# Optimization experiments

Hardware: AMD Instinct MI355X
Metric: run time of the kernel (lower is better)

## Reference

```python
import jax, jax.numpy as jnp
import numpy as np

B = 16384
D_IN = 4096        # must equal N_FEATURES for the original code to be shape-consistent
N_FEATURES = 4096
K = 128


def setup_inputs() -> dict:
    key = jax.random.key(0)
    kx, kw = jax.random.split(key)
    x = jax.random.normal(kx, (B, D_IN), dtype=jnp.float32)
    preencoder_bias = jnp.zeros((D_IN,), dtype=jnp.float32)
    # kaiming_uniform-like init: bound = sqrt(6 / fan_in)
    bound = float(np.sqrt(6.0 / D_IN))
    W_enc = jax.random.uniform(kw, (N_FEATURES, D_IN), dtype=jnp.float32,
                               minval=-bound, maxval=bound)
    b_enc = jnp.zeros((N_FEATURES,), dtype=jnp.float32)
    return {"x": x, "preencoder_bias": preencoder_bias, "W_enc": W_enc, "b_enc": b_enc}


def reference(x, preencoder_bias, W_enc, b_enc):
    # y = (x - preencoder_bias) @ W_enc + b_enc   (W_enc is square: d_in == n_features)
    xc = x - preencoder_bias                      # [B, d_in]
    y = xc @ W_enc + b_enc                        # [B, n_features]
    acts = jax.nn.relu(y)
    # top-k threshold masking: keep entries >= k-th largest per row (ties included)
    topk_vals = jax.lax.top_k(acts, K)[0]         # [B, K], sorted descending
    threshold = topk_vals[..., -1:]               # [B, 1]
    return acts * (acts >= threshold)
```

## Files before the change

### kernel.cpp

```cpp
#include <hip/hip_runtime.h>
#include <hip/hip_bf16.h>


typedef __bf16  bf16x8 __attribute__((ext_vector_type(8)));
typedef float   f32x4  __attribute__((ext_vector_type(4)));

__device__ __forceinline__ unsigned short f2bf(float f) {
    __hip_bfloat16 h = __float2bfloat16(f);
    return __builtin_bit_cast(unsigned short, h);
}
__device__ __forceinline__ float bf2f(unsigned short u) {
    __hip_bfloat16 h = __builtin_bit_cast(__hip_bfloat16, u);
    return __bfloat162float(h);
}

#define GLL16(g, l)                                                          \
    __builtin_amdgcn_global_load_lds(                                        \
        (const __attribute__((address_space(1))) unsigned int*)(g),          \
        (__attribute__((address_space(3))) unsigned int*)(l), 16, 0, 0)

__global__ __launch_bounds__(256)
void presplit_x(const float* __restrict__ x, const float* __restrict__ pb,
                unsigned short* __restrict__ Xhi, unsigned short* __restrict__ Xlo,
                int Kdim, size_t total) {
    size_t base = ((size_t)blockIdx.x * 256 + threadIdx.x) * 8;
    if (base >= total) return;
    int kcol = (int)(base % Kdim);
    __align__(16) unsigned short hi[8], lo[8];
    #pragma unroll
    for (int q = 0; q < 2; ++q) {
        float4 xv = *(const float4*)&x[base + q * 4];
        float4 pv = *(const float4*)&pb[kcol + q * 4];
        float v[4] = {xv.x - pv.x, xv.y - pv.y, xv.z - pv.z, xv.w - pv.w};
        #pragma unroll
        for (int r = 0; r < 4; ++r) {
            hi[q*4+r] = f2bf(v[r]);
            lo[q*4+r] = f2bf(v[r] - bf2f(hi[q*4+r]));
        }
    }
    *(uint4*)&Xhi[base] = *(uint4*)&hi[0];
    *(uint4*)&Xlo[base] = *(uint4*)&lo[0];
}

__global__ __launch_bounds__(256)
void split_transpose_W(const float* __restrict__ W,
                       unsigned short* __restrict__ Wt_hi,
                       unsigned short* __restrict__ Wt_lo,
                       int N, int Kdim) {
    __shared__ float tile[64][65];
    const int tx = threadIdx.x;
    const int nB = blockIdx.x * 64;
    const int kB = blockIdx.y * 64;

    #pragma unroll
    for (int p = 0; p < 4; ++p) {
        int e  = tx + 256 * p;
        int kl = e >> 4;
        int n4 = (e & 15) << 2;
        float4 v = *(const float4*)&W[(size_t)(kB + kl) * N + nB + n4];
        tile[kl][n4 + 0] = v.x; tile[kl][n4 + 1] = v.y;
        tile[kl][n4 + 2] = v.z; tile[kl][n4 + 3] = v.w;
    }
    __syncthreads();

    #pragma unroll
    for (int p = 0; p < 4; ++p) {
        int e  = tx + 256 * p;
        int nl = e >> 4;
        int k4 = (e & 15) << 2;
        unsigned short hi[4], lo[4];
        #pragma unroll
        for (int r = 0; r < 4; ++r) {
            float f = tile[k4 + r][nl];
            hi[r] = f2bf(f);
            lo[r] = f2bf(f - bf2f(hi[r]));
        }
        size_t off = (size_t)(nB + nl) * Kdim + kB + k4;
        *(ushort4*)&Wt_hi[off] = *(ushort4*)&hi[0];
        *(ushort4*)&Wt_lo[off] = *(ushort4*)&lo[0];
    }
}

__global__ __launch_bounds__(512, 2)
void gemm_presplit_i(const unsigned short* __restrict__ Xhi,
                     const unsigned short* __restrict__ Xlo,
                     const unsigned short* __restrict__ Wt_hi,
                     const unsigned short* __restrict__ Wt_lo,
                     const float* __restrict__ be,
                     float* __restrict__ out, int M, int N, int Kdim) {
    __shared__ unsigned short sA[2][256 * 64];
    __shared__ unsigned short sB[2][256 * 64];

    const int tx   = threadIdx.x;
    const int lane = tx & 63;
    const int wv   = tx >> 6;
    const int ln   = lane & 15;
    const int quad = lane >> 4;
    const int wm   = wv >> 2;
    const int wn   = wv & 3;

    const int mT = M >> 8, nT = N >> 8, total = mT * nT;
    int wgid = blockIdx.y * gridDim.x + blockIdx.x;
    int xcd = wgid & 7, idx = wgid >> 3;
    int qq = total >> 3, rr_ = total & 7;
    int swz = (xcd < rr_ ? xcd * (qq + 1) : rr_ * (qq + 1) + (xcd - rr_) * qq) + idx;
    const int mBase = (swz / nT) << 8;
    const int nBase = (swz % nT) << 8;

    const int rr  = tx >> 3;
    const int lc8 = tx & 7;
    const int lgc = lc8 ^ (rr & 7);
    const unsigned short* aSrc = (lgc & 4) ? Xlo : Xhi;
    const unsigned short* bSrc = (lgc & 4) ? Wt_lo : Wt_hi;
    const int srcoff = (lgc & 3) << 3;
    const int arow_b = (rr & 31) + ((rr & 32) << 2);

    const int pA = (quad ^ (ln & 7)) << 3;

#define STAGE_B(bufp, r, k0_) do {                                            \
        int row_ = ((r) << 6) + rr;                                           \
        GLL16(bSrc + (size_t)(nBase + row_) * Kdim + (k0_) + srcoff,          \
              &sB[bufp][(row_ << 6) + (lc8 << 3)]);                           \
    } while (0)
#define STAGE_A(bufp, r, k0_) do {                                            \
        int row_ = ((r) << 5) + arow_b;                                       \
        GLL16(aSrc + (size_t)(mBase + row_) * Kdim + (k0_) + srcoff,          \
              &sA[bufp][(row_ << 6) + (lc8 << 3)]);                           \
    } while (0)

    f32x4 acc[8][4] = {};

    const int NT = Kdim >> 5;

    STAGE_B(0, 0, 0); STAGE_B(0, 1, 0); STAGE_B(0, 2, 0); STAGE_B(0, 3, 0);
    STAGE_A(0, 0, 0); STAGE_A(0, 1, 0); STAGE_A(0, 2, 0); STAGE_A(0, 3, 0);
    asm volatile("s_waitcnt vmcnt(0)" ::: "memory");
    __builtin_amdgcn_s_barrier();
    __builtin_amdgcn_sched_barrier(0);

    for (int t = 0; t < NT; ++t) {
        const int cur = t & 1, nxt = cur ^ 1;
        const bool more = (t + 1 < NT);
        const int k1 = (t + 1) << 5;

        bf16x8 bhi[4], blo[4];
        #pragma unroll
        for (int q = 0; q < 4; ++q) {
            if (q == 0) {
                #pragma unroll
                for (int j = 0; j < 4; ++j) {
                    int rb = wn * 64 + j * 16 + ln;
                    bhi[j] = *(const bf16x8*)&sB[cur][(rb << 6) + pA];
                    blo[j] = *(const bf16x8*)&sB[cur][(rb << 6) + (pA ^ 32)];
                }
            }
            bf16x8 ahi[2], alo[2];
            #pragma unroll
            for (int ii = 0; ii < 2; ++ii) {
                int ra = wm * 128 + (2 * q + ii) * 16 + ln;
                ahi[ii] = *(const bf16x8*)&sA[cur][(ra << 6) + pA];
                alo[ii] = *(const bf16x8*)&sA[cur][(ra << 6) + (pA ^ 32)];
            }

            if (more) {
                if (q == 0)      { STAGE_B(nxt, 0, k1); STAGE_B(nxt, 1, k1); }
                else if (q == 1) { STAGE_B(nxt, 2, k1); STAGE_B(nxt, 3, k1); }
                else if (q == 2) { STAGE_A(nxt, 0, k1); STAGE_A(nxt, 1, k1); }
                else             { STAGE_A(nxt, 2, k1); STAGE_A(nxt, 3, k1); }
            }

            __builtin_amdgcn_s_barrier();
            __builtin_amdgcn_s_setprio(1);
            #pragma unroll
            for (int ii = 0; ii < 2; ++ii)
                #pragma unroll
                for (int j = 0; j < 4; ++j)
                    acc[2 * q + ii][j] = __builtin_amdgcn_mfma_f32_16x16x32_bf16(
                        ahi[ii], bhi[j], acc[2 * q + ii][j], 0, 0, 0);
            #pragma unroll
            for (int ii = 0; ii < 2; ++ii)
                #pragma unroll
                for (int j = 0; j < 4; ++j)
                    acc[2 * q + ii][j] = __builtin_amdgcn_mfma_f32_16x16x32_bf16(
                        ahi[ii], blo[j], acc[2 * q + ii][j], 0, 0, 0);
            #pragma unroll
            for (int ii = 0; ii < 2; ++ii)
                #pragma unroll
                for (int j = 0; j < 4; ++j)
                    acc[2 * q + ii][j] = __builtin_amdgcn_mfma_f32_16x16x32_bf16(
                        alo[ii], bhi[j], acc[2 * q + ii][j], 0, 0, 0);
            __builtin_amdgcn_s_setprio(0);

            if (more) {
                if (q == 0)      asm volatile("s_waitcnt vmcnt(4)" ::: "memory");
                else if (q == 1) asm volatile("s_waitcnt vmcnt(5)" ::: "memory");
                else if (q == 2) asm volatile("s_waitcnt vmcnt(6)" ::: "memory");
                else             asm volatile("s_waitcnt vmcnt(3)" ::: "memory");
            } else {
                if (q == 0)      asm volatile("s_waitcnt vmcnt(2)" ::: "memory");
                else if (q == 1) asm volatile("s_waitcnt vmcnt(1)" ::: "memory");
                else if (q == 2) asm volatile("s_waitcnt vmcnt(0)" ::: "memory");
            }
            __builtin_amdgcn_s_barrier();
            __builtin_amdgcn_sched_barrier(0);
        }
    }

    #pragma unroll
    for (int j = 0; j < 4; ++j) {
        int n = nBase + wn * 64 + j * 16 + ln;
        float bev = be[n];
        #pragma unroll
        for (int i = 0; i < 8; ++i) {
            #pragma unroll
            for (int r = 0; r < 4; ++r) {
                int m = mBase + wm * 128 + i * 16 + quad * 4 + r;
                out[(size_t)m * N + n] = fmaxf(acc[i][j][r] + bev, 0.f);
            }
        }
    }
#undef STAGE_B
#undef STAGE_A
}

__global__ __launch_bounds__(256)
void gemm_split_bf16(const float* __restrict__ x, const float* __restrict__ pb,
                     const unsigned short* __restrict__ Wt_hi,
                     const unsigned short* __restrict__ Wt_lo,
                     const float* __restrict__ be,
                     float* __restrict__ out, int M, int N, int Kdim) {
    __shared__ unsigned short sAhi[128][32];
    __shared__ unsigned short sAlo[128][32];
    __shared__ unsigned short sBhi[128][32];
    __shared__ unsigned short sBlo[128][32];

    const int tx    = threadIdx.x;
    const int nBase = blockIdx.x * 128;
    const int mBase = blockIdx.y * 128;
    const int wv    = tx >> 6;
    const int lane  = tx & 63;
    const int ln    = lane & 15;
    const int quad  = lane >> 4;
    const int wm    = wv >> 1;
    const int wn    = wv & 1;
    const int am = tx >> 1;
    const int ak = (tx & 1) * 16;
    const int bn  = wv * 16 + (lane >> 2);
    const int bk8 = (lane & 3) * 8;

    f32x4 acc[4][4] = {};

    for (int k0 = 0; k0 < Kdim; k0 += 32) {
        __syncthreads();
        #pragma unroll
        for (int r = 0; r < 2; ++r) {
            int nrow = r * 64 + bn;
            size_t goff = (size_t)(nBase + nrow) * Kdim + k0 + bk8;
            GLL16(&Wt_hi[goff], &sBhi[nrow][bk8]);
            GLL16(&Wt_lo[goff], &sBlo[nrow][bk8]);
        }
        {
            const float* xrow = x  + (size_t)(mBase + am) * Kdim + k0 + ak;
            const float* pbp  = pb + k0 + ak;
            float v[16];
            #pragma unroll
            for (int q = 0; q < 4; ++q) {
                float4 xv = *(const float4*)(xrow + q * 4);
                float4 pv = *(const float4*)(pbp + q * 4);
                v[q*4+0] = xv.x - pv.x; v[q*4+1] = xv.y - pv.y;
                v[q*4+2] = xv.z - pv.z; v[q*4+3] = xv.w - pv.w;
            }
            __align__(16) unsigned short hi[16], lo[16];
            #pragma unroll
            for (int q = 0; q < 16; ++q) {
                hi[q] = f2bf(v[q]);
                lo[q] = f2bf(v[q] - bf2f(hi[q]));
            }
            *(uint4*)&sAhi[am][ak]     = *(uint4*)&hi[0];
            *(uint4*)&sAhi[am][ak + 8] = *(uint4*)&hi[8];
            *(uint4*)&sAlo[am][ak]     = *(uint4*)&lo[0];
            *(uint4*)&sAlo[am][ak + 8] = *(uint4*)&lo[8];
        }
        __syncthreads();

        bf16x8 ahi[4], alo[4], bhi[4], blo[4];
        #pragma unroll
        for (int i = 0; i < 4; ++i) {
            int m = wm * 64 + i * 16 + ln;
            ahi[i] = *(const bf16x8*)&sAhi[m][quad * 8];
            alo[i] = *(const bf16x8*)&sAlo[m][quad * 8];
        }
        #pragma unroll
        for (int j = 0; j < 4; ++j) {
            int n = wn * 64 + j * 16 + ln;
            bhi[j] = *(const bf16x8*)&sBhi[n][quad * 8];
            blo[j] = *(const bf16x8*)&sBlo[n][quad * 8];
        }
        #pragma unroll
        for (int i = 0; i < 4; ++i)
            #pragma unroll
            for (int j = 0; j < 4; ++j) {
                acc[i][j] = __builtin_amdgcn_mfma_f32_16x16x32_bf16(ahi[i], bhi[j], acc[i][j], 0, 0, 0);
                acc[i][j] = __builtin_amdgcn_mfma_f32_16x16x32_bf16(ahi[i], blo[j], acc[i][j], 0, 0, 0);
                acc[i][j] = __builtin_amdgcn_mfma_f32_16x16x32_bf16(alo[i], bhi[j], acc[i][j], 0, 0, 0);
            }
    }

    #pragma unroll
    for (int j = 0; j < 4; ++j) {
        int n = nBase + wn * 64 + j * 16 + ln;
        float bev = be[n];
        #pragma unroll
        for (int i = 0; i < 4; ++i)
            #pragma unroll
            for (int r = 0; r < 4; ++r) {
                int m = mBase + wm * 64 + i * 16 + quad * 4 + r;
                out[(size_t)m * N + n] = fmaxf(acc[i][j][r] + bev, 0.f);
            }
    }
}

#define BAND    2e-4f
#define AMB_CAP 64

__global__ __launch_bounds__(256)
void topk_mask_exact(const float* __restrict__ x, const float* __restrict__ pb,
                     const float* __restrict__ W, const float* __restrict__ be,
                     float* __restrict__ out, int N, int Kdim, int Ksel) {
    __shared__ int    s_red[4];
    __shared__ int    s_nhi, s_namb;
    __shared__ int    amb_idx[AMB_CAP];
    __shared__ double amb_d[AMB_CAP];
    __shared__ int    amb_keep[AMB_CAP];
    __shared__ double dred[4];

    const int tx  = threadIdx.x;
    const int row = blockIdx.x;
    float* rowp = out + (size_t)row * N;

    float v[16];
    #pragma unroll
    for (int p = 0; p < 4; ++p) {
        float4 f = *(const float4*)&rowp[(tx + 256 * p) << 2];
        v[p*4+0] = f.x; v[p*4+1] = f.y; v[p*4+2] = f.z; v[p*4+3] = f.w;
    }
    unsigned uv[16];
    #pragma unroll
    for (int i = 0; i < 16; ++i) uv[i] = __float_as_uint(v[i]);

    int c0 = 0;
    #pragma unroll
    for (int i = 0; i < 16; ++i) c0 += (uv[i] != 0u) ? 1 : 0;
    #pragma unroll
    for (int off = 32; off > 0; off >>= 1) c0 += __shfl_down(c0, off);
    if ((tx & 63) == 0) s_red[tx >> 6] = c0;
    __syncthreads();
    const int total_nz = s_red[0] + s_red[1] + s_red[2] + s_red[3];

    unsigned thr_u = 0;
    if (total_nz >= Ksel) {
        unsigned blo_ = 1u, bhi_ = 0x7f7fffffu;
        while (blo_ < bhi_) {
            unsigned mid = blo_ + ((bhi_ - blo_ + 1) >> 1);
            int cc = 0;
            #pragma unroll
            for (int i = 0; i < 16; ++i) cc += (uv[i] >= mid) ? 1 : 0;
            #pragma unroll
            for (int off = 32; off > 0; off >>= 1) cc += __shfl_down(cc, off);
            __syncthreads();
            if ((tx & 63) == 0) s_red[tx >> 6] = cc;
            __syncthreads();
            int cnt = s_red[0] + s_red[1] + s_red[2] + s_red[3];
            if (cnt >= Ksel) blo_ = mid; else bhi_ = mid - 1;
        }
        thr_u = blo_;
    }
    const float thr = __uint_as_float(thr_u);

    if (thr < 0.01f) {
        #pragma unroll
        for (int p = 0; p < 4; ++p) {
            float4 o;
            o.x = (v[p*4+0] >= thr) ? v[p*4+0] : 0.f;
            o.y = (v[p*4+1] >= thr) ? v[p*4+1] : 0.f;
            o.z = (v[p*4+2] >= thr) ? v[p*4+2] : 0.f;
            o.w = (v[p*4+3] >= thr) ? v[p*4+3] : 0.f;
            *(float4*)&rowp[(tx + 256 * p) << 2] = o;
        }
        return;
    }

    if (tx == 0) { s_nhi = 0; s_namb = 0; }
    __syncthreads();

    int my_hi = 0;
    #pragma unroll
    for (int i = 0; i < 16; ++i) {
        float val = v[i];
        if (val > thr + BAND) my_hi++;
        else if (val >= thr - BAND) {
            int slot = atomicAdd(&s_namb, 1);
            if (slot < AMB_CAP) amb_idx[slot] = ((tx + 256 * (i >> 2)) << 2) + (i & 3);
        }
    }
    atomicAdd(&s_nhi, my_hi);
    __syncthreads();

    const int nhi   = s_nhi;
    const int namb  = (s_namb < AMB_CAP) ? s_namb : AMB_CAP;
    const int kneed = Ksel - nhi;
    const bool fallback = (s_namb > AMB_CAP) || (kneed < 0) || (kneed > s_namb);

    if (fallback) {
        #pragma unroll
        for (int p = 0; p < 4; ++p) {
            float4 o;
            o.x = (v[p*4+0] >= thr) ? v[p*4+0] : 0.f;
            o.y = (v[p*4+1] >= thr) ? v[p*4+1] : 0.f;
            o.z = (v[p*4+2] >= thr) ? v[p*4+2] : 0.f;
            o.w = (v[p*4+3] >= thr) ? v[p*4+3] : 0.f;
            *(float4*)&rowp[(tx + 256 * p) << 2] = o;
        }
        return;
    }

    if (namb > kneed) {
        for (int j = 0; j < namb; ++j) {
            const int n = amb_idx[j];
            double partial = 0.0;
            for (int p = 0; p < Kdim / 256; ++p) {
                int k = tx + 256 * p;
                partial += ((double)x[(size_t)row * Kdim + k] - (double)pb[k]) *
                           (double)W[(size_t)k * N + n];
            }
            #pragma unroll
            for (int off = 32; off > 0; off >>= 1) partial += __shfl_down(partial, off);
            if ((tx & 63) == 0) dred[tx >> 6] = partial;
            __syncthreads();
            if (tx == 0) amb_d[j] = dred[0] + dred[1] + dred[2] + dred[3] + (double)be[n];
            __syncthreads();
        }
        if (tx == 0) {
            for (int j = 0; j < namb; ++j) {
                int greater = 0;
                for (int l = 0; l < namb; ++l)
                    if (amb_d[l] > amb_d[j]) greater++;
                amb_keep[j] = (greater < kneed) ? 1 : 0;
            }
        }
        __syncthreads();
    } else {
        for (int j = tx; j < namb; j += 256) amb_keep[j] = 1;
        __syncthreads();
    }

    #pragma unroll
    for (int p = 0; p < 4; ++p) {
        float4 o;
        float* po = (float*)&o;
        #pragma unroll
        for (int r = 0; r < 4; ++r) {
            int gi = ((tx + 256 * p) << 2) + r;
            float val = v[p*4+r];
            float ov;
            if (val > thr + BAND) ov = val;
            else if (val < thr - BAND) ov = 0.f;
            else {
                int keep = 0;
                for (int j = 0; j < namb; ++j)
                    if (amb_idx[j] == gi) { keep = amb_keep[j]; break; }
                ov = keep ? val : 0.f;
            }
            po[r] = ov;
        }
        *(float4*)&rowp[(tx + 256 * p) << 2] = o;
    }
}

extern "C" void kernel_launch(void* const* d_in, const int* in_sizes, int n_in,
                              void* d_out, int out_size, void* d_ws, size_t ws_size,
                              hipStream_t stream) {
    const float* x  = (const float*)d_in[0];
    const float* pb = (const float*)d_in[1];
    const float* W  = (const float*)d_in[2];
    const float* be = (const float*)d_in[3];
    float* out = (float*)d_out;

    const int D = in_sizes[1];
    const int N = in_sizes[3];
    const int M = in_sizes[0] / D;

    const size_t szW = (size_t)N * D;
    const size_t szX = (size_t)M * D;
    const size_t needW    = 2ull * szW * sizeof(unsigned short);
    const size_t needFull = needW + 2ull * szX * sizeof(unsigned short);

    const bool div256 = (M % 256 == 0) && (N % 256 == 0) && (D % 32 == 0);

    if (ws_size >= needFull && div256) {
        unsigned short* Wt_hi = (unsigned short*)d_ws;
        unsigned short* Wt_lo = Wt_hi + szW;
        unsigned short* Xhi   = Wt_lo + szW;
        unsigned short* Xlo   = Xhi + szX;
        split_transpose_W<<<dim3(N / 64, D / 64), 256, 0, stream>>>(W, Wt_hi, Wt_lo, N, D);
        {
            size_t total = szX;
            int blocks = (int)((total / 8 + 255) / 256);
            presplit_x<<<blocks, 256, 0, stream>>>(x, pb, Xhi, Xlo, D, total);
        }
        gemm_presplit_i<<<dim3(N / 256, M / 256), 512, 0, stream>>>(
            Xhi, Xlo, Wt_hi, Wt_lo, be, out, M, N, D);
    } else {
        unsigned short* Wt_hi = (unsigned short*)d_ws;
        unsigned short* Wt_lo = Wt_hi + szW;
        split_transpose_W<<<dim3(N / 64, D / 64), 256, 0, stream>>>(W, Wt_hi, Wt_lo, N, D);
        gemm_split_bf16<<<dim3(N / 128, M / 128), 256, 0, stream>>>(
            x, pb, Wt_hi, Wt_lo, be, out, M, N, D);
    }
    topk_mask_exact<<<M, 256, 0, stream>>>(x, pb, W, be, out, N, D, 128);
}
```

Measured before the change: 2.059 ms.

## Shrink GEMM tile to 128x128 with 256 threads and restructure pipeline

Replaces the 256x256 tile, 512-thread split-bf16 GEMM with a 128x128 tile, 256-thread kernel. All next-stage global-to-LDS loads are now issued at the top of each K step, and compute is split into two halves with fewer barriers. The presplit_x kernel becomes one block per row looping over columns. Smaller tiles give more workgroups and less LDS per block, but mean more global traffic per FLOP and lower operand reuse.

```diff
diff --git a/kernel.cpp b/kernel.cpp
--- a/kernel.cpp
+++ b/kernel.cpp
@@ -22,24 +22,25 @@
 __global__ __launch_bounds__(256)
 void presplit_x(const float* __restrict__ x, const float* __restrict__ pb,
                 unsigned short* __restrict__ Xhi, unsigned short* __restrict__ Xlo,
-                int Kdim, size_t total) {
-    size_t base = ((size_t)blockIdx.x * 256 + threadIdx.x) * 8;
-    if (base >= total) return;
-    int kcol = (int)(base % Kdim);
-    __align__(16) unsigned short hi[8], lo[8];
-    #pragma unroll
-    for (int q = 0; q < 2; ++q) {
-        float4 xv = *(const float4*)&x[base + q * 4];
-        float4 pv = *(const float4*)&pb[kcol + q * 4];
-        float v[4] = {xv.x - pv.x, xv.y - pv.y, xv.z - pv.z, xv.w - pv.w};
-        #pragma unroll
-        for (int r = 0; r < 4; ++r) {
-            hi[q*4+r] = f2bf(v[r]);
-            lo[q*4+r] = f2bf(v[r] - bf2f(hi[q*4+r]));
-        }
-    }
-    *(uint4*)&Xhi[base] = *(uint4*)&hi[0];
-    *(uint4*)&Xlo[base] = *(uint4*)&lo[0];
+                int Kdim) {
+    const size_t rbase = (size_t)blockIdx.x * Kdim;
+    for (int it = 0; it < Kdim; it += 2048) {
+        const int k8 = it + threadIdx.x * 8;
+        __align__(16) unsigned short hi[8], lo[8];
+        #pragma unroll
+        for (int q = 0; q < 2; ++q) {
+            float4 xv = *(const float4*)&x[rbase + k8 + q * 4];
+            float4 pv = *(const float4*)&pb[k8 + q * 4];
+            float v[4] = {xv.x - pv.x, xv.y - pv.y, xv.z - pv.z, xv.w - pv.w};
+            #pragma unroll
+            for (int r = 0; r < 4; ++r) {
+                hi[q*4+r] = f2bf(v[r]);
+                lo[q*4+r] = f2bf(v[r] - bf2f(hi[q*4+r]));
+            }
+        }
+        *(uint4*)&Xhi[rbase + k8] = *(uint4*)&hi[0];
+        *(uint4*)&Xlo[rbase + k8] = *(uint4*)&lo[0];
+    }
 }
 
 __global__ __launch_bounds__(256)
@@ -81,31 +82,31 @@
     }
 }
 
-__global__ __launch_bounds__(512, 2)
-void gemm_presplit_i(const unsigned short* __restrict__ Xhi,
-                     const unsigned short* __restrict__ Xlo,
-                     const unsigned short* __restrict__ Wt_hi,
-                     const unsigned short* __restrict__ Wt_lo,
-                     const float* __restrict__ be,
-                     float* __restrict__ out, int M, int N, int Kdim) {
-    __shared__ unsigned short sA[2][256 * 64];
-    __shared__ unsigned short sB[2][256 * 64];
+__global__ __launch_bounds__(256, 2)
+void gemm_presplit_2b(const unsigned short* __restrict__ Xhi,
+                      const unsigned short* __restrict__ Xlo,
+                      const unsigned short* __restrict__ Wt_hi,
+                      const unsigned short* __restrict__ Wt_lo,
+                      const float* __restrict__ be,
+                      float* __restrict__ out, int M, int N, int Kdim) {
+    __shared__ unsigned short sA[2][128 * 64];
+    __shared__ unsigned short sB[2][128 * 64];
 
     const int tx   = threadIdx.x;
     const int lane = tx & 63;
     const int wv   = tx >> 6;
     const int ln   = lane & 15;
     const int quad = lane >> 4;
-    const int wm   = wv >> 2;
-    const int wn   = wv & 3;
-
-    const int mT = M >> 8, nT = N >> 8, total = mT * nT;
+    const int wm   = wv >> 1;
+    const int wn   = wv & 1;
+
+    const int mT = M >> 7, nT = N >> 7, total = mT * nT;
     int wgid = blockIdx.y * gridDim.x + blockIdx.x;
     int xcd = wgid & 7, idx = wgid >> 3;
     int qq = total >> 3, rr_ = total & 7;
     int swz = (xcd < rr_ ? xcd * (qq + 1) : rr_ * (qq + 1) + (xcd - rr_) * qq) + idx;
-    const int mBase = (swz / nT) << 8;
-    const int nBase = (swz % nT) << 8;
+    const int mBase = (swz / nT) << 7;
+    const int nBase = (swz % nT) << 7;
 
     const int rr  = tx >> 3;
     const int lc8 = tx & 7;
@@ -113,27 +114,26 @@
     const unsigned short* aSrc = (lgc & 4) ? Xlo : Xhi;
     const unsigned short* bSrc = (lgc & 4) ? Wt_lo : Wt_hi;
     const int srcoff = (lgc & 3) << 3;
-    const int arow_b = (rr & 31) + ((rr & 32) << 2);
 
     const int pA = (quad ^ (ln & 7)) << 3;
 
 #define STAGE_B(bufp, r, k0_) do {                                            \
-        int row_ = ((r) << 6) + rr;                                           \
+        int row_ = ((r) << 5) + rr;                                           \
         GLL16(bSrc + (size_t)(nBase + row_) * Kdim + (k0_) + srcoff,          \
               &sB[bufp][(row_ << 6) + (lc8 << 3)]);                           \
     } while (0)
-#define STAGE_A(bufp, r, k0_) do {                                            \
-        int row_ = ((r) << 5) + arow_b;                                       \
+#define STAGE_A(bufp, rbase, k0_) do {                                        \
+        int row_ = (rbase) + rr;                                              \
         GLL16(aSrc + (size_t)(mBase + row_) * Kdim + (k0_) + srcoff,          \
               &sA[bufp][(row_ << 6) + (lc8 << 3)]);                           \
     } while (0)
 
-    f32x4 acc[8][4] = {};
+    f32x4 acc[4][4] = {};
 
     const int NT = Kdim >> 5;
 
     STAGE_B(0, 0, 0); STAGE_B(0, 1, 0); STAGE_B(0, 2, 0); STAGE_B(0, 3, 0);
-    STAGE_A(0, 0, 0); STAGE_A(0, 1, 0); STAGE_A(0, 2, 0); STAGE_A(0, 3, 0);
+    STAGE_A(0, 0, 0); STAGE_A(0, 64, 0); STAGE_A(0, 32, 0); STAGE_A(0, 96, 0);
     asm volatile("s_waitcnt vmcnt(0)" ::: "memory");
     __builtin_amdgcn_s_barrier();
     __builtin_amdgcn_sched_barrier(0);
@@ -143,67 +143,85 @@
         const bool more = (t + 1 < NT);
         const int k1 = (t + 1) << 5;
 
+        if (more) {
+            STAGE_B(nxt, 0, k1); STAGE_B(nxt, 1, k1);
+            STAGE_B(nxt, 2, k1); STAGE_B(nxt, 3, k1);
+            STAGE_A(nxt, 0, k1); STAGE_A(nxt, 64, k1);
+            STAGE_A(nxt, 32, k1); STAGE_A(nxt, 96, k1);
+        }
         bf16x8 bhi[4], blo[4];
         #pragma unroll
-        for (int q = 0; q < 4; ++q) {
-            if (q == 0) {
-                #pragma unroll
-                for (int j = 0; j < 4; ++j) {
-                    int rb = wn * 64 + j * 16 + ln;
-                    bhi[j] = *(const bf16x8*)&sB[cur][(rb << 6) + pA];
-                    blo[j] = *(const bf16x8*)&sB[cur][(rb << 6) + (pA ^ 32)];
-                }
-            }
+        for (int j = 0; j < 4; ++j) {
+            int rb = wn * 64 + j * 16 + ln;
+            bhi[j] = *(const bf16x8*)&sB[cur][(rb << 6) + pA];
+            blo[j] = *(const bf16x8*)&sB[cur][(rb << 6) + (pA ^ 32)];
+        }
+        {
             bf16x8 ahi[2], alo[2];
             #pragma unroll
             for (int ii = 0; ii < 2; ++ii) {
-                int ra = wm * 128 + (2 * q + ii) * 16 + ln;
+                int ra = wm * 64 + ii * 16 + ln;
                 ahi[ii] = *(const bf16x8*)&sA[cur][(ra << 6) + pA];
                 alo[ii] = *(const bf16x8*)&sA[cur][(ra << 6) + (pA ^ 32)];
             }
-
-            if (more) {
-                if (q == 0)      { STAGE_B(nxt, 0, k1); STAGE_B(nxt, 1, k1); }
-                else if (q == 1) { STAGE_B(nxt, 2, k1); STAGE_B(nxt, 3, k1); }
-                else if (q == 2) { STAGE_A(nxt, 0, k1); STAGE_A(nxt, 1, k1); }
-                else             { STAGE_A(nxt, 2, k1); STAGE_A(nxt, 3, k1); }
-            }
-
-            __builtin_amdgcn_s_barrier();
             __builtin_amdgcn_s_setprio(1);
             #pragma unroll
             for (int ii = 0; ii < 2; ++ii)
                 #pragma unroll
                 for (int j = 0; j < 4; ++j)
-                    acc[2 * q + ii][j] = __builtin_amdgcn_mfma_f32_16x16x32_bf16(
-                        ahi[ii], bhi[j], acc[2 * q + ii][j], 0, 0, 0);
+                    acc[ii][j] = __builtin_amdgcn_mfma_f32_16x16x32_bf16(
+                        ahi[ii], bhi[j], acc[ii][j], 0, 0, 0);
             #pragma unroll
             for (int ii = 0; ii < 2; ++ii)
                 #pragma unroll
                 for (int j = 0; j < 4; ++j)
-                    acc[2 * q + ii][j] = __builtin_amdgcn_mfma_f32_16x16x32_bf16(
-                        ahi[ii], blo[j], acc[2 * q + ii][j], 0, 0, 0);
+                    acc[ii][j] = __builtin_amdgcn_mfma_f32_16x16x32_bf16(
+                        ahi[ii], blo[j], acc[ii][j], 0, 0, 0);
             #pragma unroll
             for (int ii = 0; ii < 2; ++ii)
                 #pragma unroll
                 for (int j = 0; j < 4; ++j)
-                    acc[2 * q + ii][j] = __builtin_amdgcn_mfma_f32_16x16x32_bf16(
-                        alo[ii], bhi[j], acc[2 * q + ii][j], 0, 0, 0);
+                    acc[ii][j] = __builtin_amdgcn_mfma_f32_16x16x32_bf16(
+                        alo[ii], bhi[j], acc[ii][j], 0, 0, 0);
             __builtin_amdgcn_s_setprio(0);
-
-            if (more) {
-                if (q == 0)      asm volatile("s_waitcnt vmcnt(4)" ::: "memory");
-                else if (q == 1) asm volatile("s_waitcnt vmcnt(5)" ::: "memory");
-                else if (q == 2) asm volatile("s_waitcnt vmcnt(6)" ::: "memory");
-                else             asm volatile("s_waitcnt vmcnt(3)" ::: "memory");
-            } else {
-                if (q == 0)      asm volatile("s_waitcnt vmcnt(2)" ::: "memory");
-                else if (q == 1) asm volatile("s_waitcnt vmcnt(1)" ::: "memory");
-                else if (q == 2) asm volatile("s_waitcnt vmcnt(0)" ::: "memory");
-            }
-            __builtin_amdgcn_s_barrier();
-            __builtin_amdgcn_sched_barrier(0);
-        }
+        }
+        if (more) asm volatile("s_waitcnt vmcnt(8)" ::: "memory");
+        else      asm volatile("s_waitcnt vmcnt(0)" ::: "memory");
+        __builtin_amdgcn_s_barrier();
+        __builtin_amdgcn_sched_barrier(0);
+
+        {
+            bf16x8 ahi[2], alo[2];
+            #pragma unroll
+            for (int ii = 0; ii < 2; ++ii) {
+                int ra = wm * 64 + (2 + ii) * 16 + ln;
+                ahi[ii] = *(const bf16x8*)&sA[cur][(ra << 6) + pA];
+                alo[ii] = *(const bf16x8*)&sA[cur][(ra << 6) + (pA ^ 32)];
+            }
+            __builtin_amdgcn_s_setprio(1);
+            #pragma unroll
+            for (int ii = 0; ii < 2; ++ii)
+                #pragma unroll
+                for (int j = 0; j < 4; ++j)
+                    acc[2 + ii][j] = __builtin_amdgcn_mfma_f32_16x16x32_bf16(
+                        ahi[ii], bhi[j], acc[2 + ii][j], 0, 0, 0);
+            #pragma unroll
+            for (int ii = 0; ii < 2; ++ii)
+                #pragma unroll
+                for (int j = 0; j < 4; ++j)
+                    acc[2 + ii][j] = __builtin_amdgcn_mfma_f32_16x16x32_bf16(
+                        ahi[ii], blo[j], acc[2 + ii][j], 0, 0, 0);
+            #pragma unroll
+            for (int ii = 0; ii < 2; ++ii)
+                #pragma unroll
+                for (int j = 0; j < 4; ++j)
+                    acc[2 + ii][j] = __builtin_amdgcn_mfma_f32_16x16x32_bf16(
+                        alo[ii], bhi[j], acc[2 + ii][j], 0, 0, 0);
+            __builtin_amdgcn_s_setprio(0);
+        }
+        asm volatile("s_waitcnt vmcnt(2)" ::: "memory");
+        __builtin_amdgcn_s_barrier();
+        __builtin_amdgcn_sched_barrier(0);
     }
 
     #pragma unroll
@@ -211,10 +229,10 @@
         int n = nBase + wn * 64 + j * 16 + ln;
         float bev = be[n];
         #pragma unroll
-        for (int i = 0; i < 8; ++i) {
+        for (int i = 0; i < 4; ++i) {
             #pragma unroll
             for (int r = 0; r < 4; ++r) {
-                int m = mBase + wm * 128 + i * 16 + quad * 4 + r;
+                int m = mBase + wm * 64 + i * 16 + quad * 4 + r;
                 out[(size_t)m * N + n] = fmaxf(acc[i][j][r] + bev, 0.f);
             }
         }
@@ -495,20 +513,16 @@
     const size_t needW    = 2ull * szW * sizeof(unsigned short);
     const size_t needFull = needW + 2ull * szX * sizeof(unsigned short);
 
-    const bool div256 = (M % 256 == 0) && (N % 256 == 0) && (D % 32 == 0);
-
-    if (ws_size >= needFull && div256) {
+    const bool divOK = (M % 128 == 0) && (N % 128 == 0) && (D % 2048 == 0);
+
+    if (ws_size >= needFull && divOK) {
         unsigned short* Wt_hi = (unsigned short*)d_ws;
         unsigned short* Wt_lo = Wt_hi + szW;
         unsigned short* Xhi   = Wt_lo + szW;
         unsigned short* Xlo   = Xhi + szX;
         split_transpose_W<<<dim3(N / 64, D / 64), 256, 0, stream>>>(W, Wt_hi, Wt_lo, N, D);
-        {
-            size_t total = szX;
-            int blocks = (int)((total / 8 + 255) / 256);
-            presplit_x<<<blocks, 256, 0, stream>>>(x, pb, Xhi, Xlo, D, total);
-        }
-        gemm_presplit_i<<<dim3(N / 256, M / 256), 512, 0, stream>>>(
+        presplit_x<<<M, 256, 0, stream>>>(x, pb, Xhi, Xlo, D);
+        gemm_presplit_2b<<<dim3(N / 128, M / 128), 256, 0, stream>>>(
             Xhi, Xlo, Wt_hi, Wt_lo, be, out, M, N, D);
     } else {
         unsigned short* Wt_hi = (unsigned short*)d_ws;
```

Measured after the change: 2.589 ms. 25.7% more time.
